# Performance work log

Hardware: AMD Instinct MI355X
Metric: run time of the kernel (lower is better)

The kernel has to match this reference:

```python
import jax, jax.numpy as jnp
import numpy as np

N = 100000      # total nodes = B_GRAPHS * NODES_PER_GRAPH
NPG = 1000      # nodes per graph (num_nodes in module)
B_GRAPHS = 100
H = 128         # hidden_channels
CIN = 3         # in_channels
E = 1600000     # edges (avg_degree 16)
OUT = 2         # out_channels


def setup_inputs() -> dict:
    key = jax.random.key(0)
    ks = jax.random.split(key, 20)
    s = 0.05
    inp = {
        "x": jax.random.normal(ks[0], (N, CIN), jnp.float32),
        "edge_index": jnp.stack([
            jax.random.randint(ks[1], (E,), 0, N),
            jax.random.randint(ks[2], (E,), 0, N),
        ]).astype(jnp.int64),
        "batch": jnp.repeat(jnp.arange(B_GRAPHS), NPG).astype(jnp.int64),
        # DiffusionConv layer 0: CIN -> H ; layer 1: H -> H
        "W_self0": jax.random.normal(ks[3], (CIN, H), jnp.float32) * s,
        "W_nbr0": jax.random.normal(ks[4], (CIN, H), jnp.float32) * s,
        "b0": jnp.zeros((H,), jnp.float32),
        "W_self1": jax.random.normal(ks[5], (H, H), jnp.float32) * s,
        "W_nbr1": jax.random.normal(ks[6], (H, H), jnp.float32) * s,
        "b1": jnp.zeros((H,), jnp.float32),
        # 2 stacked LSTMs (torch layout: W_ih [4H, in], W_hh [4H, H])
        "Wih0": jax.random.normal(ks[7], (4 * H, H), jnp.float32) * s,
        "Whh0": jax.random.normal(ks[8], (4 * H, H), jnp.float32) * s,
        "bih0": jnp.zeros((4 * H,), jnp.float32),
        "bhh0": jnp.zeros((4 * H,), jnp.float32),
        "Wih1": jax.random.normal(ks[9], (4 * H, H), jnp.float32) * s,
        "Whh1": jax.random.normal(ks[10], (4 * H, H), jnp.float32) * s,
        "bih1": jnp.zeros((4 * H,), jnp.float32),
        "bhh1": jnp.zeros((4 * H,), jnp.float32),
        # output head
        "W_out": jax.random.normal(ks[11], (H, OUT), jnp.float32) * s,
        "b_out": jnp.zeros((OUT,), jnp.float32),
    }
    return inp


def diffusion_conv(h, src, dst, W_self, W_nbr, b):
    # gather-aggregate-transform: out = h W_self + (D^-1 A h) W_nbr + b
    msgs = h[src]                                            # [E, C] gather
    agg = jax.ops.segment_sum(msgs, dst, num_segments=N)     # [N, C] scatter-add
    deg = jax.ops.segment_sum(jnp.ones((src.shape[0], 1), h.dtype), dst,
                              num_segments=N)                # [N, 1]
    agg = agg / jnp.maximum(deg, 1.0)
    return h @ W_self + agg @ W_nbr + b


def lstm_layer(x_seq, Wih, Whh, bih, bhh):
    # x_seq: [T, Bn, H] seq-first, zero initial state (torch default)
    Bn = x_seq.shape[1]
    h0 = jnp.zeros((Bn, H), x_seq.dtype)
    c0 = jnp.zeros((Bn, H), x_seq.dtype)

    def step(carry, xt):
        h, c = carry
        g = xt @ Wih.T + h @ Whh.T + (bih + bhh)   # [Bn, 4H]
        i, f, gg, o = jnp.split(g, 4, axis=-1)     # torch gate order i,f,g,o
        c = jax.nn.sigmoid(f) * c + jax.nn.sigmoid(i) * jnp.tanh(gg)
        h = jax.nn.sigmoid(o) * jnp.tanh(c)
        return (h, c), h

    _, hs = jax.lax.scan(step, (h0, c0), x_seq)
    return hs


def reference(x, edge_index, batch, W_self0, W_nbr0, b0, W_self1, W_nbr1, b1,
              Wih0, Whh0, bih0, bhh0, Wih1, Whh1, bih1, bhh1, W_out, b_out):
    src, dst = edge_index[0], edge_index[1]
    h = jax.nn.relu(diffusion_conv(x, src, dst, W_self0, W_nbr0, b0))
    h = jax.nn.relu(diffusion_conv(h, src, dst, W_self1, W_nbr1, b1))
    # view(-1, num_nodes, hidden): [B_GRAPHS, NPG, H], LSTM seq-first
    seq = h.reshape(B_GRAPHS, NPG, H)
    seq = lstm_layer(seq, Wih0, Whh0, bih0, bhh0)
    seq = lstm_layer(seq, Wih1, Whh1, bih1, bhh1)
    h = seq.reshape(N, H)
    # global_mean_pool over batch vector
    pooled = jax.ops.segment_sum(h, batch, num_segments=B_GRAPHS)
    cnt = jax.ops.segment_sum(jnp.ones((N, 1), h.dtype), batch,
                              num_segments=B_GRAPHS)
    pooled = pooled / jnp.maximum(cnt, 1.0)
    logits = pooled @ W_out + b_out                # [B_GRAPHS, OUT]
    return jax.nn.log_softmax(logits, axis=1)
```

## Files before the change

### kernel.cpp

```cpp
#include <hip/hip_runtime.h>

#define N_NODES 100000
#define NPG     1000
#define B_GR    100
#define HDIM    128
#define E_EDGES 1600000

typedef __attribute__((ext_vector_type(8))) short bf16x8;
typedef __attribute__((ext_vector_type(4))) float f32x4;
typedef unsigned long long u64;
typedef unsigned short u16;

__device__ __forceinline__ float sigf(float x) { return 1.f / (1.f + __expf(-x)); }
__device__ __forceinline__ float tanh_fast(float x) { return 1.f - 2.f / (__expf(2.f * x) + 1.f); }
__device__ __forceinline__ u16 f2bf(float f) {
    unsigned u = __float_as_uint(f);
    unsigned r = (u + 0x7fffu + ((u >> 16) & 1u)) >> 16;
    return (u16)r;
}
__device__ __forceinline__ float bf2f(u16 h) { return __uint_as_float(((unsigned)h) << 16); }
__device__ __forceinline__ f32x4 MF(bf16x8 a, bf16x8 b, f32x4 c) {
    return __builtin_amdgcn_mfma_f32_16x16x32_bf16(a, b, c, 0, 0, 0);
}
__device__ __forceinline__ u64 pack4(f32x4 a) {
    return (u64)f2bf(a[0]) | ((u64)f2bf(a[1]) << 16)
         | ((u64)f2bf(a[2]) << 32) | ((u64)f2bf(a[3]) << 48);
}
#define BAR() asm volatile("s_waitcnt lgkmcnt(0)\n\ts_barrier" ::: "memory")

__global__ void k_build(const int* __restrict__ src, const int* __restrict__ dst,
                        int* __restrict__ cnt, int* __restrict__ ell) {
    int e = blockIdx.x * 256 + threadIdx.x;
    if (e >= E_EDGES) return;
    int d = dst[e];
    int pos = atomicAdd(&cnt[d], 1);
    if (pos < 64) ell[(size_t)d * 64 + pos] = src[e];
}

__global__ __launch_bounds__(256)
void k_conv0w(const float* __restrict__ x, const int* __restrict__ cnt, const int* __restrict__ ell,
              const float* __restrict__ Ws, const float* __restrict__ Wn, const float* __restrict__ b,
              u16* __restrict__ Hbf) {
    int n = blockIdx.x * 4 + (threadIdx.x >> 6);
    int lane = threadIdx.x & 63;
    if (n >= N_NODES) return;
    int degt = cnt[n];
    int deg = min(degt, 64);
    float a0 = 0.f, a1 = 0.f, a2 = 0.f;
    if (lane < deg) {
        int s = ell[(size_t)n * 64 + lane];
        a0 = x[s * 3 + 0]; a1 = x[s * 3 + 1]; a2 = x[s * 3 + 2];
    }
#pragma unroll
    for (int off = 1; off < 64; off <<= 1) {
        a0 += __shfl_xor(a0, off);
        a1 += __shfl_xor(a1, off);
        a2 += __shfl_xor(a2, off);
    }
    float inv = 1.f / fmaxf((float)degt, 1.f);
    a0 *= inv; a1 *= inv; a2 *= inv;
    float x0 = x[n * 3 + 0], x1 = x[n * 3 + 1], x2 = x[n * 3 + 2];
#pragma unroll
    for (int q = 0; q < 2; ++q) {
        int c = lane + 64 * q;
        float acc = b[c]
            + x0 * Ws[c] + x1 * Ws[128 + c] + x2 * Ws[256 + c]
            + a0 * Wn[c] + a1 * Wn[128 + c] + a2 * Wn[256 + c];
        Hbf[(size_t)n * 128 + c] = f2bf(fmaxf(acc, 0.f));
    }
}

__global__ __launch_bounds__(256)
void k_agg2e(const u16* __restrict__ hin, const int* __restrict__ cnt, const int* __restrict__ ell,
             u16* __restrict__ out) {
    int wid = threadIdx.x >> 6;
    int l = threadIdx.x & 63;
    int n = blockIdx.x * 4 + wid;
    if (n >= N_NODES) return;
    int degt = cnt[n];
    int deg = min(degt, 64);
    int myidx = ell[(size_t)n * 64 + l];
    float ax = 0.f, ay = 0.f;
    const unsigned* base = (const unsigned*)hin;
    int j = 0;
    for (; j + 4 <= deg; j += 4) {
        int i0 = __shfl(myidx, j);
        int i1 = __shfl(myidx, j + 1);
        int i2 = __shfl(myidx, j + 2);
        int i3 = __shfl(myidx, j + 3);
        unsigned v0 = base[(size_t)i0 * 64 + l];
        unsigned v1 = base[(size_t)i1 * 64 + l];
        unsigned v2 = base[(size_t)i2 * 64 + l];
        unsigned v3 = base[(size_t)i3 * 64 + l];
        ax += bf2f((u16)v0); ay += bf2f((u16)(v0 >> 16));
        ax += bf2f((u16)v1); ay += bf2f((u16)(v1 >> 16));
        ax += bf2f((u16)v2); ay += bf2f((u16)(v2 >> 16));
        ax += bf2f((u16)v3); ay += bf2f((u16)(v3 >> 16));
    }
    for (; j < deg; ++j) {
        int i0 = __shfl(myidx, j);
        unsigned v = base[(size_t)i0 * 64 + l];
        ax += bf2f((u16)v); ay += bf2f((u16)(v >> 16));
    }
    float dv = fmaxf((float)degt, 1.f);
    unsigned o = (unsigned)f2bf(ax / dv) | ((unsigned)f2bf(ay / dv) << 16);
    *(unsigned*)&out[(size_t)n * 128 + l * 2] = o;
}

__global__ void k_prepc(const float* __restrict__ Wself, const float* __restrict__ Wnbr,
                        u16* __restrict__ WCf) {
    int idx = blockIdx.x * 256 + threadIdx.x;
    int fi = idx & 4095;
    int lo = idx >> 12;
    int lane = fi & 63;
    int colt = (fi >> 6) & 7;
    int kt = fi >> 9;
    int col = colt * 16 + (lane & 15);
    int k0 = kt * 32 + (lane >> 4) * 8;
    u16 o[8];
#pragma unroll
    for (int j = 0; j < 8; ++j) {
        int k = k0 + j;
        float v = (k < 128) ? Wself[k * 128 + col] : Wnbr[(k - 128) * 128 + col];
        u16 hi = f2bf(v);
        o[j] = lo ? f2bf(v - bf2f(hi)) : hi;
    }
    u64* dst = (u64*)(WCf + (size_t)idx * 8);
    dst[0] = (u64)o[0] | ((u64)o[1] << 16) | ((u64)o[2] << 32) | ((u64)o[3] << 48);
    dst[1] = (u64)o[4] | ((u64)o[5] << 16) | ((u64)o[6] << 32) | ((u64)o[7] << 48);
}

__global__ __launch_bounds__(256, 1)
void k_conv1f(const u16* __restrict__ Hbf, const u16* __restrict__ AGbf,
              const u16* __restrict__ WCf, const float* __restrict__ bias,
              u16* __restrict__ Xf) {
    extern __shared__ __align__(16) u16 smem[];
    int tid = threadIdx.x;
    int l = tid & 63, w = tid >> 6;
    {
        const u64* Wsrc = (const u64*)WCf;
        u64* Wd = (u64*)smem;
#pragma unroll
        for (int i = 0; i < 64; ++i)
            Wd[tid + 256 * i] = Wsrc[tid + 256 * i];
    }
    __syncthreads();
    int r0 = blockIdx.x * 256 + w * 64;

#pragma unroll 1
    for (int g = 0; g < 4; ++g) {
        int rowA = r0 + g * 16 + (l & 15);
        int row = min(rowA, N_NODES - 1);
        int koff = (l >> 4) * 8;
        bf16x8 act[8];
#pragma unroll
        for (int kt = 0; kt < 4; ++kt) {
            act[kt]     = *(const bf16x8*)(Hbf  + (size_t)row * 128 + kt * 32 + koff);
            act[4 + kt] = *(const bf16x8*)(AGbf + (size_t)row * 128 + kt * 32 + koff);
        }
        f32x4 acc[8];
#pragma unroll
        for (int c = 0; c < 8; ++c) acc[c] = (f32x4){0.f, 0.f, 0.f, 0.f};
#pragma unroll
        for (int kt = 0; kt < 8; ++kt)
#pragma unroll
            for (int colt = 0; colt < 8; ++colt) {
                bf16x8 wf = *(const bf16x8*)(smem + ((kt * 8 + colt) * 64 + l) * 8);
                acc[colt] = MF(wf, act[kt], acc[colt]);
            }
#pragma unroll
        for (int kt = 0; kt < 8; ++kt)
#pragma unroll
            for (int colt = 0; colt < 8; ++colt) {
                bf16x8 wf = *(const bf16x8*)(smem + 32768 + ((kt * 8 + colt) * 64 + l) * 8);
                acc[colt] = MF(wf, act[kt], acc[colt]);
            }
        if (rowA < N_NODES) {
            int t = rowA / 1000;
            int rv = rowA - t * 1000;
            int rb2 = rv >> 4, rr = rv & 15;
            size_t tilebase = (size_t)(t * 63 + rb2) * 2048 + rr * 8;
#pragma unroll
            for (int colt = 0; colt < 8; ++colt) {
                int col0 = colt * 16 + ((l >> 4) << 2);
                f32x4 v;
#pragma unroll
                for (int reg = 0; reg < 4; ++reg)
                    v[reg] = fmaxf(acc[colt][reg] + bias[col0 + reg], 0.f);
                size_t idx = tilebase + (size_t)((col0 >> 5) * 512 + ((col0 >> 3) & 3) * 128 + (col0 & 7));
                *(u64*)(Xf + idx) = pack4(v);
            }
        }
    }
}

__global__ void k_prepf(const float* __restrict__ Wih0, const float* __restrict__ Whh0,
                        const float* __restrict__ Wih1, const float* __restrict__ Whh1,
                        u16* __restrict__ WTf) {
    int idx = blockIdx.x * 256 + threadIdx.x;
    int lane = idx & 63;
    int gt = (idx >> 6) & 3;
    int kt = (idx >> 8) & 7;
    int w  = (idx >> 11) & 7;
    int l  = idx >> 14;
    int d = 16 * w + (lane & 15);
    int k0 = kt * 32 + (lane >> 4) * 8;
    int wrow = gt * 128 + d;
    const float* Wi = l ? Wih1 : Wih0;
    const float* Wh = l ? Whh1 : Whh0;
    const float* srcp = (k0 < 128) ? (Wi + wrow * 128 + k0) : (Wh + wrow * 128 + (k0 - 128));
    u16 o[8];
#pragma unroll
    for (int j = 0; j < 8; ++j) o[j] = f2bf(srcp[j]);
    u64* dst = (u64*)(WTf + (size_t)idx * 8);
    dst[0] = (u64)o[0] | ((u64)o[1] << 16) | ((u64)o[2] << 32) | ((u64)o[3] << 48);
    dst[1] = (u64)o[4] | ((u64)o[5] << 16) | ((u64)o[6] << 32) | ((u64)o[7] << 48);
}

__global__ void k_bsum(const float* __restrict__ bih0, const float* __restrict__ bhh0,
                       const float* __restrict__ bih1, const float* __restrict__ bhh1,
                       float* __restrict__ bs) {
    int i = blockIdx.x * 256 + threadIdx.x;
    int l = i >> 9, c = i & 511;
    bs[i] = l ? (bih1[c] + bhh1[c]) : (bih0[c] + bhh0[c]);
}

__global__ __launch_bounds__(512, 1)
void k_gemmA(const u16* __restrict__ src, const u16* __restrict__ WTf,
             const float* __restrict__ bsB, u16* __restrict__ Gx, int t0, int layer) {
    extern __shared__ __align__(16) u16 smem[];
    int tid = threadIdx.x;
    int l = tid & 63, w = tid >> 6;
    int rb = blockIdx.x % 63;
    int slice = blockIdx.x / 63;
    int nt = (slice < 2) ? 13 : 12;
    int ts = (slice < 2) ? slice * 13 : 26 + (slice - 2) * 12;
    {
        const u64* Wsrc = (const u64*)(WTf + (size_t)layer * 131072);
        u64* Wd = (u64*)smem;
#pragma unroll
        for (int i = 0; i < 32; ++i) {
            int j = tid + i * 512;
            int dfrag = j >> 7, r = j & 127;
            int w_ = dfrag >> 4, kt2 = (dfrag >> 2) & 3, gt = dfrag & 3;
            int gfrag = (w_ * 8 + kt2) * 4 + gt;
            Wd[j] = Wsrc[(size_t)gfrag * 128 + r];
        }
    }
    __syncthreads();
    int d = (w << 4) | (l & 15);
    float b0v = bsB[layer * 512 + d];
    float b1v = bsB[layer * 512 + 128 + d];
    float b2v = bsB[layer * 512 + 256 + d];
    float b3v = bsB[layer * 512 + 384 + d];
    const u16* wbase = smem + (size_t)w * 8192 + l * 8;
    for (int tt = 0; tt < nt; ++tt) {
        int tc = ts + tt;
        int t = t0 + tc;
        const u16* xb = src + ((size_t)t * 63 + rb) * 2048 + l * 8;
        bf16x8 x0 = *(const bf16x8*)(xb);
        bf16x8 x1 = *(const bf16x8*)(xb + 512);
        bf16x8 x2 = *(const bf16x8*)(xb + 1024);
        bf16x8 x3 = *(const bf16x8*)(xb + 1536);
        f32x4 a0 = {b0v, b0v, b0v, b0v};
        f32x4 a1 = {b1v, b1v, b1v, b1v};
        f32x4 a2 = {b2v, b2v, b2v, b2v};
        f32x4 a3 = {b3v, b3v, b3v, b3v};
#pragma unroll
        for (int kt2 = 0; kt2 < 4; ++kt2) {
            bf16x8 xa = (kt2 == 0) ? x0 : (kt2 == 1) ? x1 : (kt2 == 2) ? x2 : x3;
            a0 = MF(xa, *(const bf16x8*)(wbase + (kt2 * 4 + 0) * 512), a0);
            a1 = MF(xa, *(const bf16x8*)(wbase + (kt2 * 4 + 1) * 512), a1);
            a2 = MF(xa, *(const bf16x8*)(wbase + (kt2 * 4 + 2) * 512), a2);
            a3 = MF(xa, *(const bf16x8*)(wbase + (kt2 * 4 + 3) * 512), a3);
        }
        size_t gbase = ((size_t)tc * 63 + rb) * 8192 + (size_t)w * 1024 + l * 4;
        *(u64*)(Gx + gbase)       = pack4(a0);
        *(u64*)(Gx + gbase + 256) = pack4(a1);
        *(u64*)(Gx + gbase + 512) = pack4(a2);
        *(u64*)(Gx + gbase + 768) = pack4(a3);
    }
}

__global__ __launch_bounds__(512, 1)
void k_recB(const u16* __restrict__ Gx, const u16* __restrict__ WTf,
            u16* __restrict__ H0f, float* __restrict__ pooled,
            u16* __restrict__ hstate, float* __restrict__ cstate,
            int t0, int layer) {
    extern __shared__ __align__(16) u16 smem[];
    u16* Wlds = smem;
    u16* hshA = smem + 65536;
    u16* hshB = smem + 67584;
    int tid = threadIdx.x;
    int l = tid & 63, w = tid >> 6;
    int rb = blockIdx.x;

    {
        u64 hv = (t0 == 0) ? 0ull : ((const u64*)(hstate + (size_t)rb * 2048))[tid];
        ((u64*)hshA)[tid] = hv;
    }
    {
        const u64* Wsrc = (const u64*)(WTf + (size_t)layer * 131072);
        u64* Wd = (u64*)Wlds;
#pragma unroll
        for (int i = 0; i < 32; ++i) {
            int j = tid + i * 512;
            int dfrag = j >> 7, r = j & 127;
            int w_ = dfrag >> 4, kt2 = (dfrag >> 2) & 3, gt = dfrag & 3;
            int gfrag = (w_ * 8 + 4 + kt2) * 4 + gt;
            Wd[j] = Wsrc[(size_t)gfrag * 128 + r];
        }
    }
    float cst0, cst1, cst2, cst3;
    if (t0 == 0) {
        cst0 = cst1 = cst2 = cst3 = 0.f;
    } else {
        const f32x4 cv = *(const f32x4*)(cstate + ((size_t)rb * 512 + tid) * 4);
        cst0 = cv[0]; cst1 = cv[1]; cst2 = cv[2]; cst3 = cv[3];
    }
    __syncthreads();

    int d = (w << 4) | (l & 15);
    int ktp = d >> 5, oct = (d >> 3) & 3, boff = d & 7;
    int hbase = ktp * 512 + ((l >> 4) * 4 + 16 * oct) * 8 + boff;
    const u16* wbase = Wlds + (size_t)w * 8192 + l * 8;
    int n0 = rb * 16;
    int nreal = min(16, NPG - n0);
    int cur = 0;

    size_t goff = (size_t)w * 1024 + l * 4;
    const u64* g0p = (const u64*)(Gx + (size_t)rb * 8192 + goff);
    u64 p0 = g0p[0], p1 = g0p[32], p2 = g0p[64], p3 = g0p[96];

    for (int tt = 0; tt < 50; ++tt) {
        int t = t0 + tt;
        const u16* hc = cur ? hshB : hshA;
        u16* hn = cur ? hshA : hshB;
        f32x4 a0 = {0.f, 0.f, 0.f, 0.f};
        f32x4 a1 = {0.f, 0.f, 0.f, 0.f};
        f32x4 a2 = {0.f, 0.f, 0.f, 0.f};
        f32x4 a3 = {0.f, 0.f, 0.f, 0.f};
#pragma unroll
        for (int kt2 = 0; kt2 < 4; ++kt2) {
            bf16x8 hf = *(const bf16x8*)(hc + kt2 * 512 + l * 8);
            a0 = MF(hf, *(const bf16x8*)(wbase + (kt2 * 4 + 0) * 512), a0);
            a1 = MF(hf, *(const bf16x8*)(wbase + (kt2 * 4 + 1) * 512), a1);
            a2 = MF(hf, *(const bf16x8*)(wbase + (kt2 * 4 + 2) * 512), a2);
            a3 = MF(hf, *(const bf16x8*)(wbase + (kt2 * 4 + 3) * 512), a3);
        }
        u64 q0 = 0, q1 = 0, q2 = 0, q3 = 0;
        if (tt < 49) {
            const u64* gp = (const u64*)(Gx + ((size_t)(tt + 1) * 63 + rb) * 8192 + goff);
            q0 = gp[0]; q1 = gp[32]; q2 = gp[64]; q3 = gp[96];
        }
        float hsum = 0.f;
#pragma unroll
        for (int reg = 0; reg < 4; ++reg) {
            float gi = a0[reg] + bf2f((u16)(p0 >> (16 * reg)));
            float gf = a1[reg] + bf2f((u16)(p1 >> (16 * reg)));
            float gg = a2[reg] + bf2f((u16)(p2 >> (16 * reg)));
            float go = a3[reg] + bf2f((u16)(p3 >> (16 * reg)));
            float cprev = (reg == 0) ? cst0 : (reg == 1) ? cst1 : (reg == 2) ? cst2 : cst3;
            float c = sigf(gf) * cprev + sigf(gi) * tanh_fast(gg);
            if (reg == 0) cst0 = c; else if (reg == 1) cst1 = c;
            else if (reg == 2) cst2 = c; else cst3 = c;
            float h = sigf(go) * tanh_fast(c);
            u16 hb = f2bf(h);
            hn[hbase + reg * 8] = hb;
            if (layer == 0) {
                H0f[((size_t)t * 63 + rb) * 2048 + hbase + reg * 8] = hb;
            } else {
                int row = (l >> 4) * 4 + reg;
                if (row < nreal) hsum += h;
            }
        }
        if (layer == 1) {
            hsum += __shfl_xor(hsum, 16);
            hsum += __shfl_xor(hsum, 32);
            if ((l >> 4) == 0) atomicAdd(&pooled[t * 128 + d], hsum);
        }
        BAR();
        p0 = q0; p1 = q1; p2 = q2; p3 = q3;
        cur ^= 1;
    }
    ((u64*)(hstate + (size_t)rb * 2048))[tid] = ((const u64*)(cur ? hshB : hshA))[tid];
    f32x4 cv = {cst0, cst1, cst2, cst3};
    *(f32x4*)(cstate + ((size_t)rb * 512 + tid) * 4) = cv;
}

__global__ void k_head(const float* __restrict__ pooled, const float* __restrict__ Wout,
                       const float* __restrict__ bout, float* __restrict__ out) {
    int gi = threadIdx.x;
    if (gi >= B_GR) return;
    float l0 = bout[0], l1 = bout[1];
    for (int d = 0; d < 128; ++d) {
        float p = pooled[gi * 128 + d] / 1000.0f;
        l0 += p * Wout[d * 2 + 0];
        l1 += p * Wout[d * 2 + 1];
    }
    float m = fmaxf(l0, l1);
    float lse = m + logf(__expf(l0 - m) + __expf(l1 - m));
    out[gi * 2 + 0] = l0 - lse;
    out[gi * 2 + 1] = l1 - lse;
}

extern "C" void kernel_launch(void* const* d_in, const int* in_sizes, int n_in,
                              void* d_out, int out_size, void* d_ws, size_t ws_size,
                              hipStream_t stream) {
    const float* x    = (const float*)d_in[0];
    const int*   ei   = (const int*)d_in[1];
    const int*   srcI = ei;
    const int*   dstI = ei + E_EDGES;
    const float* Ws0  = (const float*)d_in[3];
    const float* Wn0  = (const float*)d_in[4];
    const float* b0   = (const float*)d_in[5];
    const float* Ws1  = (const float*)d_in[6];
    const float* Wn1  = (const float*)d_in[7];
    const float* b1   = (const float*)d_in[8];
    const float* Wih0 = (const float*)d_in[9];
    const float* Whh0 = (const float*)d_in[10];
    const float* bih0 = (const float*)d_in[11];
    const float* bhh0 = (const float*)d_in[12];
    const float* Wih1 = (const float*)d_in[13];
    const float* Whh1 = (const float*)d_in[14];
    const float* bih1 = (const float*)d_in[15];
    const float* bhh1 = (const float*)d_in[16];
    const float* Wout = (const float*)d_in[17];
    const float* bout = (const float*)d_in[18];
    float* out = (float*)d_out;

    char* ws = (char*)d_ws;
    int*   cnt    = (int*)(ws + 0);
    int*   ell    = (int*)(ws + 400128);
    u16*   Hbf    = (u16*)(ws + 26000128);
    u16*   AGbf   = (u16*)(ws + 51600128);
    u16*   Xf     = (u16*)(ws + 77414400);
    u16*   WTf    = (u16*)(ws + 103219200);
    float* bsB    = (float*)(ws + 103743488);
    float* pooled = (float*)(ws + 103747584);
    u16*   hstate = (u16*)(ws + 103798784);
    float* cstate = (float*)(ws + 104056832);
    u16*   WCf    = (u16*)(ws + 104572928);
    u16*   H0f    = (u16*)(ws + 0);
    u16*   Gx     = (u16*)(ws + 25804800);

    hipMemsetAsync(cnt, 0, 400128, stream);
    hipMemsetAsync(pooled, 0, B_GR * 128 * sizeof(float), stream);

    k_build<<<E_EDGES / 256, 256, 0, stream>>>(srcI, dstI, cnt, ell);
    k_conv0w<<<N_NODES / 4, 256, 0, stream>>>(x, cnt, ell, Ws0, Wn0, b0, Hbf);
    k_agg2e<<<N_NODES / 4, 256, 0, stream>>>(Hbf, cnt, ell, AGbf);
    k_prepc<<<32, 256, 0, stream>>>(Ws1, Wn1, WCf);

    hipFuncSetAttribute((const void*)k_conv1f, hipFuncAttributeMaxDynamicSharedMemorySize, 131072);
    hipFuncSetAttribute((const void*)k_gemmA,  hipFuncAttributeMaxDynamicSharedMemorySize, 131072);
    hipFuncSetAttribute((const void*)k_recB,   hipFuncAttributeMaxDynamicSharedMemorySize, 139264);

    k_conv1f<<<(N_NODES + 255) / 256, 256, 131072, stream>>>(Hbf, AGbf, WCf, b1, Xf);

    k_prepf<<<128, 256, 0, stream>>>(Wih0, Whh0, Wih1, Whh1, WTf);
    k_bsum<<<4, 256, 0, stream>>>(bih0, bhh0, bih1, bhh1, bsB);

    for (int layer = 0; layer < 2; ++layer) {
        const u16* srcT = layer ? H0f : Xf;
        for (int half = 0; half < 2; ++half) {
            int t0 = half * 50;
            k_gemmA<<<252, 512, 131072, stream>>>(srcT, WTf, bsB, Gx, t0, layer);
            k_recB<<<63, 512, 139264, stream>>>(Gx, WTf, H0f, pooled, hstate, cstate, t0, layer);
        }
    }

    k_head<<<1, 128, 0, stream>>>(pooled, Wout, bout, out);
}
```

Baseline: 847.7 us.

## Fuse LSTM input GEMM and recurrence into one persistent flag-synchronized pipeline kernel

Replaces the eight alternating gemmA/recB launches with a single persistent kernel of 252 blocks split into four roles: input-projection producer and recurrent consumer for each of the two LSTM layers. They communicate through 8-slot fp32 ring buffers and per-row-block atomic flags with release/acquire fences, so both layers run concurrently in a wavefront. This removes launch gaps, the hstate/cstate save and restore, and the serialization between layers. In exchange it depends on all 252 blocks being co-resident, otherwise the spin-waits deadlock. It also adds flag polling latency and doubles gate-buffer traffic by storing fp32 instead of bf16.

New measurement: 2.293 ms. 170% more time.

```diff
diff --git a/kernel.cpp b/kernel.cpp
--- a/kernel.cpp
+++ b/kernel.cpp
@@ -26,7 +26,6 @@
     return (u64)f2bf(a[0]) | ((u64)f2bf(a[1]) << 16)
          | ((u64)f2bf(a[2]) << 32) | ((u64)f2bf(a[3]) << 48);
 }
-#define BAR() asm volatile("s_waitcnt lgkmcnt(0)\n\ts_barrier" ::: "memory")
 
 __global__ void k_build(const int* __restrict__ src, const int* __restrict__ dst,
                         int* __restrict__ cnt, int* __restrict__ ell) {
@@ -226,97 +225,39 @@
 }
 
 __global__ __launch_bounds__(512, 1)
-void k_gemmA(const u16* __restrict__ src, const u16* __restrict__ WTf,
-             const float* __restrict__ bsB, u16* __restrict__ Gx, int t0, int layer) {
+void k_lstm_pipe(const u16* __restrict__ Xf, const u16* __restrict__ WTf,
+                 const float* __restrict__ bsB, u16* __restrict__ H0f,
+                 float* __restrict__ Gx0, float* __restrict__ G1,
+                 float* __restrict__ pooled, int* __restrict__ flags) {
     extern __shared__ __align__(16) u16 smem[];
+    u16* Wlds = smem;
+    u16* hshA = smem + 65536;
+    u16* hshB = smem + 67584;
+    int* fB0 = flags;
+    int* fB1 = flags + 64;
+    int* fB2 = flags + 128;
+    int* fB3 = flags + 192;
+
     int tid = threadIdx.x;
     int l = tid & 63, w = tid >> 6;
+    int role = blockIdx.x / 63;
     int rb = blockIdx.x % 63;
-    int slice = blockIdx.x / 63;
-    int nt = (slice < 2) ? 13 : 12;
-    int ts = (slice < 2) ? slice * 13 : 26 + (slice - 2) * 12;
+    int layer = role >> 1;
+    int kh = role & 1;
+
+    ((u64*)hshA)[tid] = 0ull;
+
     {
         const u64* Wsrc = (const u64*)(WTf + (size_t)layer * 131072);
-        u64* Wd = (u64*)smem;
+        u64* Wd = (u64*)Wlds;
 #pragma unroll
         for (int i = 0; i < 32; ++i) {
             int j = tid + i * 512;
             int dfrag = j >> 7, r = j & 127;
             int w_ = dfrag >> 4, kt2 = (dfrag >> 2) & 3, gt = dfrag & 3;
-            int gfrag = (w_ * 8 + kt2) * 4 + gt;
+            int gfrag = (w_ * 8 + kh * 4 + kt2) * 4 + gt;
             Wd[j] = Wsrc[(size_t)gfrag * 128 + r];
         }
-    }
-    __syncthreads();
-    int d = (w << 4) | (l & 15);
-    float b0v = bsB[layer * 512 + d];
-    float b1v = bsB[layer * 512 + 128 + d];
-    float b2v = bsB[layer * 512 + 256 + d];
-    float b3v = bsB[layer * 512 + 384 + d];
-    const u16* wbase = smem + (size_t)w * 8192 + l * 8;
-    for (int tt = 0; tt < nt; ++tt) {
-        int tc = ts + tt;
-        int t = t0 + tc;
-        const u16* xb = src + ((size_t)t * 63 + rb) * 2048 + l * 8;
-        bf16x8 x0 = *(const bf16x8*)(xb);
-        bf16x8 x1 = *(const bf16x8*)(xb + 512);
-        bf16x8 x2 = *(const bf16x8*)(xb + 1024);
-        bf16x8 x3 = *(const bf16x8*)(xb + 1536);
-        f32x4 a0 = {b0v, b0v, b0v, b0v};
-        f32x4 a1 = {b1v, b1v, b1v, b1v};
-        f32x4 a2 = {b2v, b2v, b2v, b2v};
-        f32x4 a3 = {b3v, b3v, b3v, b3v};
-#pragma unroll
-        for (int kt2 = 0; kt2 < 4; ++kt2) {
-            bf16x8 xa = (kt2 == 0) ? x0 : (kt2 == 1) ? x1 : (kt2 == 2) ? x2 : x3;
-            a0 = MF(xa, *(const bf16x8*)(wbase + (kt2 * 4 + 0) * 512), a0);
-            a1 = MF(xa, *(const bf16x8*)(wbase + (kt2 * 4 + 1) * 512), a1);
-            a2 = MF(xa, *(const bf16x8*)(wbase + (kt2 * 4 + 2) * 512), a2);
-            a3 = MF(xa, *(const bf16x8*)(wbase + (kt2 * 4 + 3) * 512), a3);
-        }
-        size_t gbase = ((size_t)tc * 63 + rb) * 8192 + (size_t)w * 1024 + l * 4;
-        *(u64*)(Gx + gbase)       = pack4(a0);
-        *(u64*)(Gx + gbase + 256) = pack4(a1);
-        *(u64*)(Gx + gbase + 512) = pack4(a2);
-        *(u64*)(Gx + gbase + 768) = pack4(a3);
-    }
-}
-
-__global__ __launch_bounds__(512, 1)
-void k_recB(const u16* __restrict__ Gx, const u16* __restrict__ WTf,
-            u16* __restrict__ H0f, float* __restrict__ pooled,
-            u16* __restrict__ hstate, float* __restrict__ cstate,
-            int t0, int layer) {
-    extern __shared__ __align__(16) u16 smem[];
-    u16* Wlds = smem;
-    u16* hshA = smem + 65536;
-    u16* hshB = smem + 67584;
-    int tid = threadIdx.x;
-    int l = tid & 63, w = tid >> 6;
-    int rb = blockIdx.x;
-
-    {
-        u64 hv = (t0 == 0) ? 0ull : ((const u64*)(hstate + (size_t)rb * 2048))[tid];
-        ((u64*)hshA)[tid] = hv;
-    }
-    {
-        const u64* Wsrc = (const u64*)(WTf + (size_t)layer * 131072);
-        u64* Wd = (u64*)Wlds;
-#pragma unroll
-        for (int i = 0; i < 32; ++i) {
-            int j = tid + i * 512;
-            int dfrag = j >> 7, r = j & 127;
-            int w_ = dfrag >> 4, kt2 = (dfrag >> 2) & 3, gt = dfrag & 3;
-            int gfrag = (w_ * 8 + 4 + kt2) * 4 + gt;
-            Wd[j] = Wsrc[(size_t)gfrag * 128 + r];
-        }
-    }
-    float cst0, cst1, cst2, cst3;
-    if (t0 == 0) {
-        cst0 = cst1 = cst2 = cst3 = 0.f;
-    } else {
-        const f32x4 cv = *(const f32x4*)(cstate + ((size_t)rb * 512 + tid) * 4);
-        cst0 = cv[0]; cst1 = cv[1]; cst2 = cv[2]; cst3 = cv[3];
     }
     __syncthreads();
 
@@ -324,68 +265,124 @@
     int ktp = d >> 5, oct = (d >> 3) & 3, boff = d & 7;
     int hbase = ktp * 512 + ((l >> 4) * 4 + 16 * oct) * 8 + boff;
     const u16* wbase = Wlds + (size_t)w * 8192 + l * 8;
-    int n0 = rb * 16;
-    int nreal = min(16, NPG - n0);
-    int cur = 0;
-
-    size_t goff = (size_t)w * 1024 + l * 4;
-    const u64* g0p = (const u64*)(Gx + (size_t)rb * 8192 + goff);
-    u64 p0 = g0p[0], p1 = g0p[32], p2 = g0p[64], p3 = g0p[96];
-
-    for (int tt = 0; tt < 50; ++tt) {
-        int t = t0 + tt;
-        const u16* hc = cur ? hshB : hshA;
-        u16* hn = cur ? hshA : hshB;
-        f32x4 a0 = {0.f, 0.f, 0.f, 0.f};
-        f32x4 a1 = {0.f, 0.f, 0.f, 0.f};
-        f32x4 a2 = {0.f, 0.f, 0.f, 0.f};
-        f32x4 a3 = {0.f, 0.f, 0.f, 0.f};
-#pragma unroll
-        for (int kt2 = 0; kt2 < 4; ++kt2) {
-            bf16x8 hf = *(const bf16x8*)(hc + kt2 * 512 + l * 8);
-            a0 = MF(hf, *(const bf16x8*)(wbase + (kt2 * 4 + 0) * 512), a0);
-            a1 = MF(hf, *(const bf16x8*)(wbase + (kt2 * 4 + 1) * 512), a1);
-            a2 = MF(hf, *(const bf16x8*)(wbase + (kt2 * 4 + 2) * 512), a2);
-            a3 = MF(hf, *(const bf16x8*)(wbase + (kt2 * 4 + 3) * 512), a3);
+    const size_t SLOT = 516096;
+    size_t gxoff = ((size_t)rb * 8 + w) * 1024 + l * 4;
+
+    if (kh == 0) {
+        float b0v = bsB[layer * 512 + d];
+        float b1v = bsB[layer * 512 + 128 + d];
+        float b2v = bsB[layer * 512 + 256 + d];
+        float b3v = bsB[layer * 512 + 384 + d];
+        const u16* src = (layer == 0) ? Xf : H0f;
+        int* wait_flag = (layer == 0) ? nullptr : fB1;
+        int* bp_flag   = (layer == 0) ? fB1 : fB3;
+        int* my_flag   = (layer == 0) ? fB0 : fB2;
+        float* ring    = (layer == 0) ? Gx0 : G1;
+        for (int t = 0; t < 100; ++t) {
+            if (tid == 0) {
+                if (wait_flag)
+                    while (__hip_atomic_load(wait_flag + rb, __ATOMIC_RELAXED, __HIP_MEMORY_SCOPE_AGENT) < t + 1)
+                        __builtin_amdgcn_s_sleep(2);
+                while (__hip_atomic_load(bp_flag + rb, __ATOMIC_RELAXED, __HIP_MEMORY_SCOPE_AGENT) < t - 7)
+                    __builtin_amdgcn_s_sleep(2);
+            }
+            __syncthreads();
+            if (layer == 1) __builtin_amdgcn_fence(__ATOMIC_ACQUIRE, "agent");
+            const u16* xb = src + ((size_t)t * 63 + rb) * 2048 + l * 8;
+            bf16x8 x0 = *(const bf16x8*)(xb);
+            bf16x8 x1 = *(const bf16x8*)(xb + 512);
+            bf16x8 x2 = *(const bf16x8*)(xb + 1024);
+            bf16x8 x3 = *(const bf16x8*)(xb + 1536);
+            f32x4 a0 = {b0v, b0v, b0v, b0v};
+            f32x4 a1 = {b1v, b1v, b1v, b1v};
+            f32x4 a2 = {b2v, b2v, b2v, b2v};
+            f32x4 a3 = {b3v, b3v, b3v, b3v};
+#pragma unroll
+            for (int kt2 = 0; kt2 < 4; ++kt2) {
+                bf16x8 xa = (kt2 == 0) ? x0 : (kt2 == 1) ? x1 : (kt2 == 2) ? x2 : x3;
+                a0 = MF(xa, *(const bf16x8*)(wbase + (kt2 * 4 + 0) * 512), a0);
+                a1 = MF(xa, *(const bf16x8*)(wbase + (kt2 * 4 + 1) * 512), a1);
+                a2 = MF(xa, *(const bf16x8*)(wbase + (kt2 * 4 + 2) * 512), a2);
+                a3 = MF(xa, *(const bf16x8*)(wbase + (kt2 * 4 + 3) * 512), a3);
+            }
+            float* gx = ring + (size_t)(t & 7) * SLOT + gxoff;
+            *(f32x4*)(gx)       = a0;
+            *(f32x4*)(gx + 256) = a1;
+            *(f32x4*)(gx + 512) = a2;
+            *(f32x4*)(gx + 768) = a3;
+            __syncthreads();
+            if (tid == 0) {
+                __builtin_amdgcn_fence(__ATOMIC_RELEASE, "agent");
+                __hip_atomic_store(my_flag + rb, t + 1, __ATOMIC_RELAXED, __HIP_MEMORY_SCOPE_AGENT);
+            }
         }
-        u64 q0 = 0, q1 = 0, q2 = 0, q3 = 0;
-        if (tt < 49) {
-            const u64* gp = (const u64*)(Gx + ((size_t)(tt + 1) * 63 + rb) * 8192 + goff);
-            q0 = gp[0]; q1 = gp[32]; q2 = gp[64]; q3 = gp[96];
+    } else {
+        int* wait_flag = (layer == 0) ? fB0 : fB2;
+        int* my_flag   = (layer == 0) ? fB1 : fB3;
+        const float* ring = (layer == 0) ? Gx0 : G1;
+        int n0 = rb * 16;
+        int nreal = min(16, NPG - n0);
+        float cst0 = 0.f, cst1 = 0.f, cst2 = 0.f, cst3 = 0.f;
+        int cur = 0;
+        for (int t = 0; t < 100; ++t) {
+            if (tid == 0)
+                while (__hip_atomic_load(wait_flag + rb, __ATOMIC_RELAXED, __HIP_MEMORY_SCOPE_AGENT) < t + 1)
+                    __builtin_amdgcn_s_sleep(2);
+            __syncthreads();
+            __builtin_amdgcn_fence(__ATOMIC_ACQUIRE, "agent");
+            const float* gx = ring + (size_t)(t & 7) * SLOT + gxoff;
+            f32x4 g0 = *(const f32x4*)(gx);
+            f32x4 g1v = *(const f32x4*)(gx + 256);
+            f32x4 g2 = *(const f32x4*)(gx + 512);
+            f32x4 g3 = *(const f32x4*)(gx + 768);
+            const u16* hc = cur ? hshB : hshA;
+            u16* hn = cur ? hshA : hshB;
+            f32x4 a0 = {0.f, 0.f, 0.f, 0.f};
+            f32x4 a1 = {0.f, 0.f, 0.f, 0.f};
+            f32x4 a2 = {0.f, 0.f, 0.f, 0.f};
+            f32x4 a3 = {0.f, 0.f, 0.f, 0.f};
+#pragma unroll
+            for (int kt2 = 0; kt2 < 4; ++kt2) {
+                bf16x8 hf = *(const bf16x8*)(hc + kt2 * 512 + l * 8);
+                a0 = MF(hf, *(const bf16x8*)(wbase + (kt2 * 4 + 0) * 512), a0);
+                a1 = MF(hf, *(const bf16x8*)(wbase + (kt2 * 4 + 1) * 512), a1);
+                a2 = MF(hf, *(const bf16x8*)(wbase + (kt2 * 4 + 2) * 512), a2);
+                a3 = MF(hf, *(const bf16x8*)(wbase + (kt2 * 4 + 3) * 512), a3);
+            }
+            float hsum = 0.f;
+#pragma unroll
+            for (int reg = 0; reg < 4; ++reg) {
+                float gi = a0[reg] + g0[reg];
+                float gf = a1[reg] + g1v[reg];
+                float gg = a2[reg] + g2[reg];
+                float go = a3[reg] + g3[reg];
+                float cprev = (reg == 0) ? cst0 : (reg == 1) ? cst1 : (reg == 2) ? cst2 : cst3;
+                float c = sigf(gf) * cprev + sigf(gi) * tanh_fast(gg);
+                if (reg == 0) cst0 = c; else if (reg == 1) cst1 = c;
+                else if (reg == 2) cst2 = c; else cst3 = c;
+                float h = sigf(go) * tanh_fast(c);
+                u16 hb = f2bf(h);
+                hn[hbase + reg * 8] = hb;
+                if (layer == 0) {
+                    H0f[((size_t)t * 63 + rb) * 2048 + hbase + reg * 8] = hb;
+                } else {
+                    int row = (l >> 4) * 4 + reg;
+                    if (row < nreal) hsum += h;
+                }
+            }
+            if (layer == 1) {
+                hsum += __shfl_xor(hsum, 16);
+                hsum += __shfl_xor(hsum, 32);
+                if ((l >> 4) == 0) atomicAdd(&pooled[t * 128 + d], hsum);
+            }
+            __syncthreads();
+            if (tid == 0) {
+                if (layer == 0) __builtin_amdgcn_fence(__ATOMIC_RELEASE, "agent");
+                __hip_atomic_store(my_flag + rb, t + 1, __ATOMIC_RELAXED, __HIP_MEMORY_SCOPE_AGENT);
+            }
+            cur ^= 1;
         }
-        float hsum = 0.f;
-#pragma unroll
-        for (int reg = 0; reg < 4; ++reg) {
-            float gi = a0[reg] + bf2f((u16)(p0 >> (16 * reg)));
-            float gf = a1[reg] + bf2f((u16)(p1 >> (16 * reg)));
-            float gg = a2[reg] + bf2f((u16)(p2 >> (16 * reg)));
-            float go = a3[reg] + bf2f((u16)(p3 >> (16 * reg)));
-            float cprev = (reg == 0) ? cst0 : (reg == 1) ? cst1 : (reg == 2) ? cst2 : cst3;
-            float c = sigf(gf) * cprev + sigf(gi) * tanh_fast(gg);
-            if (reg == 0) cst0 = c; else if (reg == 1) cst1 = c;
-            else if (reg == 2) cst2 = c; else cst3 = c;
-            float h = sigf(go) * tanh_fast(c);
-            u16 hb = f2bf(h);
-            hn[hbase + reg * 8] = hb;
-            if (layer == 0) {
-                H0f[((size_t)t * 63 + rb) * 2048 + hbase + reg * 8] = hb;
-            } else {
-                int row = (l >> 4) * 4 + reg;
-                if (row < nreal) hsum += h;
-            }
-        }
-        if (layer == 1) {
-            hsum += __shfl_xor(hsum, 16);
-            hsum += __shfl_xor(hsum, 32);
-            if ((l >> 4) == 0) atomicAdd(&pooled[t * 128 + d], hsum);
-        }
-        BAR();
-        p0 = q0; p1 = q1; p2 = q2; p3 = q3;
-        cur ^= 1;
-    }
-    ((u64*)(hstate + (size_t)rb * 2048))[tid] = ((const u64*)(cur ? hshB : hshA))[tid];
-    f32x4 cv = {cst0, cst1, cst2, cst3};
-    *(f32x4*)(cstate + ((size_t)rb * 512 + tid) * 4) = cv;
+    }
 }
 
 __global__ void k_head(const float* __restrict__ pooled, const float* __restrict__ Wout,
@@ -438,14 +435,15 @@
     u16*   WTf    = (u16*)(ws + 103219200);
     float* bsB    = (float*)(ws + 103743488);
     float* pooled = (float*)(ws + 103747584);
-    u16*   hstate = (u16*)(ws + 103798784);
-    float* cstate = (float*)(ws + 104056832);
-    u16*   WCf    = (u16*)(ws + 104572928);
+    u16*   WCf    = (u16*)(ws + 103798784);
+    int*   flags  = (int*)(ws + 104060928);
     u16*   H0f    = (u16*)(ws + 0);
-    u16*   Gx     = (u16*)(ws + 25804800);
+    float* Gx0r   = (float*)(ws + 25804800);
+    float* G1r    = (float*)(ws + 42319872);
 
     hipMemsetAsync(cnt, 0, 400128, stream);
     hipMemsetAsync(pooled, 0, B_GR * 128 * sizeof(float), stream);
+    hipMemsetAsync(flags, 0, 1024, stream);
 
     k_build<<<E_EDGES / 256, 256, 0, stream>>>(srcI, dstI, cnt, ell);
     k_conv0w<<<N_NODES / 4, 256, 0, stream>>>(x, cnt, ell, Ws0, Wn0, b0, Hbf);
@@ -453,22 +451,14 @@
     k_prepc<<<32, 256, 0, stream>>>(Ws1, Wn1, WCf);
 
     hipFuncSetAttribute((const void*)k_conv1f, hipFuncAttributeMaxDynamicSharedMemorySize, 131072);
-    hipFuncSetAttribute((const void*)k_gemmA,  hipFuncAttributeMaxDynamicSharedMemorySize, 131072);
-    hipFuncSetAttribute((const void*)k_recB,   hipFuncAttributeMaxDynamicSharedMemorySize, 139264);
+    hipFuncSetAttribute((const void*)k_lstm_pipe, hipFuncAttributeMaxDynamicSharedMemorySize, 139264);
 
     k_conv1f<<<(N_NODES + 255) / 256, 256, 131072, stream>>>(Hbf, AGbf, WCf, b1, Xf);
 
     k_prepf<<<128, 256, 0, stream>>>(Wih0, Whh0, Wih1, Whh1, WTf);
     k_bsum<<<4, 256, 0, stream>>>(bih0, bhh0, bih1, bhh1, bsB);
 
-    for (int layer = 0; layer < 2; ++layer) {
-        const u16* srcT = layer ? H0f : Xf;
-        for (int half = 0; half < 2; ++half) {
-            int t0 = half * 50;
-            k_gemmA<<<252, 512, 131072, stream>>>(srcT, WTf, bsB, Gx, t0, layer);
-            k_recB<<<63, 512, 139264, stream>>>(Gx, WTf, H0f, pooled, hstate, cstate, t0, layer);
-        }
-    }
+    k_lstm_pipe<<<252, 512, 139264, stream>>>(Xf, WTf, bsB, H0f, Gx0r, G1r, pooled, flags);
 
     k_head<<<1, 128, 0, stream>>>(pooled, Wout, bout, out);
 }
```
